# Kernel tuning notes

Hardware: AMD Instinct MI355X
Metric: run time of the kernel (lower is better)

The kernel has to match this reference:

```python
import jax, jax.numpy as jnp
import numpy as np

H = 1024        # hidden_size
NH = 16         # num_attention_heads
DH = H // NH    # head dim = 64
I = 4096        # intermediate_size
E = 8           # moe_num_experts
B, S = 2, 2048
EPS = 1e-12


def _ln(x, g, b):
    mu = jnp.mean(x, axis=-1, keepdims=True)
    var = jnp.mean(jnp.square(x - mu), axis=-1, keepdims=True)
    return (x - mu) * jax.lax.rsqrt(var + EPS) * g + b


def setup_inputs() -> dict:
    key = jax.random.key(0)
    ks = jax.random.split(key, 16)
    std = 0.02
    p = {
        "hidden_states": jax.random.normal(ks[0], (B, S, H), jnp.float32),
        "Wq": jax.random.normal(ks[1], (H, H), jnp.float32) * std,
        "bq": jnp.zeros((H,), jnp.float32),
        "Wk": jax.random.normal(ks[2], (H, H), jnp.float32) * std,
        "bk": jnp.zeros((H,), jnp.float32),
        "Wv": jax.random.normal(ks[3], (H, H), jnp.float32) * std,
        "bv": jnp.zeros((H,), jnp.float32),
        "Wao": jax.random.normal(ks[4], (H, H), jnp.float32) * std,
        "bao": jnp.zeros((H,), jnp.float32),
        "ln1_g": jnp.ones((H,), jnp.float32),
        "ln1_b": jnp.zeros((H,), jnp.float32),
        "router_w": jax.random.normal(ks[5], (H, E), jnp.float32) * std,
        "We": jax.random.normal(ks[6], (E, H, I), jnp.float32) * std,
        "be": jnp.zeros((E, I), jnp.float32),
        "Wo": jax.random.normal(ks[7], (I, H), jnp.float32) * std,
        "bo": jnp.zeros((H,), jnp.float32),
        "ln2_g": jnp.ones((H,), jnp.float32),
        "ln2_b": jnp.zeros((H,), jnp.float32),
    }
    return p


def reference(hidden_states, Wq, bq, Wk, bk, Wv, bv, Wao, bao, ln1_g, ln1_b,
              router_w, We, be, Wo, bo, ln2_g, ln2_b):
    x = hidden_states  # [B,S,H]

    def heads(t):  # [B,S,H] -> [B,NH,S,DH]
        return t.reshape(B, S, NH, DH).transpose(0, 2, 1, 3)

    q = heads(x @ Wq + bq)
    k = heads(x @ Wk + bk)
    v = heads(x @ Wv + bv)
    scores = jnp.einsum("bhqd,bhkd->bhqk", q, k) / jnp.sqrt(jnp.float32(DH))
    probs = jax.nn.softmax(scores, axis=-1)
    ctx = jnp.einsum("bhqk,bhkd->bhqd", probs, v)
    ctx = ctx.transpose(0, 2, 1, 3).reshape(B, S, H)
    attn_out = _ln(ctx @ Wao + bao + x, ln1_g, ln1_b)  # BertSelfOutput

    # ---- MoE FFN: top-1 routing, per-expert GELU MLP, shared output proj ----
    flat = attn_out.reshape(-1, H)              # [N,H]
    logits = flat @ router_w                    # [N,E]
    idx = jnp.argmax(logits, axis=-1)           # top-1 of softmax == argmax of logits
    inter = jnp.zeros((flat.shape[0], I), flat.dtype)
    for e in range(E):  # small fixed expert count
        h_e = jax.nn.gelu(flat @ We[e] + be[e], approximate=False)
        inter = jnp.where((idx == e)[:, None], h_e, inter)
    inter = inter.reshape(B, S, I)
    out = _ln(inter @ Wo + bo + attn_out, ln2_g, ln2_b)  # BertOutput
    return out
```

## Files before the change

### kernel.cpp

```cpp
#include <hip/hip_runtime.h>
#include <hip/hip_bf16.h>
#include <cstdint>

#define H_  1024
#define NH_ 16
#define DH_ 64
#define I_  4096
#define E_  8
#define B_  2
#define S_  2048
#define N_  4096
#define QKVLD 3072
#define LN_EPS 1e-12f

typedef __attribute__((ext_vector_type(4))) float f4;
typedef __attribute__((ext_vector_type(8))) short s8v;
typedef unsigned int u32;

__device__ __forceinline__ float bf2f(unsigned short u) {
  union { unsigned int i; float f; } c; c.i = ((unsigned int)u) << 16; return c.f;
}
__device__ __forceinline__ unsigned short f2bf(float f) {
  __hip_bfloat16 h = __float2bfloat16(f);
  return *reinterpret_cast<unsigned short*>(&h);
}
__device__ __forceinline__ u32 pack_bf2(float a, float b) {
  return (u32)f2bf(a) | ((u32)f2bf(b) << 16);
}
__device__ __forceinline__ float gelu_f(float x) {
  return 0.5f * x * (1.0f + erff(x * 0.70710678118f));
}
__device__ __forceinline__ void gload16(const void* g, void* l) {
  __builtin_amdgcn_global_load_lds(
      (const __attribute__((address_space(1))) void*)g,
      (__attribute__((address_space(3))) void*)l, 16, 0, 0);
}

__global__ __launch_bounds__(256) void cvt_bf16_kernel(
    const float* __restrict__ in, ushort* __restrict__ out, int n8)
{
  const int t = blockIdx.x * 256 + threadIdx.x;
  if (t >= n8) return;
  const f4 x0 = *(const f4*)(in + (size_t)t * 8);
  const f4 x1 = *(const f4*)(in + (size_t)t * 8 + 4);
  s8v o;
#pragma unroll
  for (int j = 0; j < 4; ++j) { o[j] = (short)f2bf(x0[j]); o[4 + j] = (short)f2bf(x1[j]); }
  *(s8v*)(out + (size_t)t * 8) = o;
}

__global__ __launch_bounds__(256) void transpose_cvt_kernel(
    const float* __restrict__ in, ushort* __restrict__ out, int R, int C)
{
  __shared__ float tile[32][33];
  const size_t zo = (size_t)blockIdx.z * R * C;
  const int bx = blockIdx.x << 5, by = blockIdx.y << 5;
  const int tx = threadIdx.x & 31, ty = threadIdx.x >> 5;
  const float* ip = in + zo + (size_t)by * C + bx;
#pragma unroll
  for (int i = 0; i < 4; ++i)
    tile[ty + 8 * i][tx] = ip[(size_t)(ty + 8 * i) * C + tx];
  __syncthreads();
  ushort* op = out + zo + (size_t)bx * R + by;
#pragma unroll
  for (int i = 0; i < 4; ++i)
    op[(size_t)(ty + 8 * i) * R + tx] = f2bf(tile[tx][ty + 8 * i]);
}

__global__ void concat3_kernel(const float* a, const float* b, const float* c,
                               float* __restrict__ o)
{
  const int t = blockIdx.x * 256 + threadIdx.x;
  if (t < 1024) o[t] = a[t];
  else if (t < 2048) o[t] = b[t - 1024];
  else o[t] = c[t - 2048];
}

__global__ __launch_bounds__(256) void gather_kernel(
    const ushort* __restrict__ X, const int* __restrict__ lists,
    ushort* __restrict__ Xg)
{
  const int r = (blockIdx.x << 1) + (threadIdx.x >> 7);
  const int c = (threadIdx.x & 127) << 3;
  const int tok = lists[r];
  *(s8v*)&Xg[(size_t)r * H_ + c] = *(const s8v*)&X[(size_t)tok * H_ + c];
}

template <bool BF16OUT, int KSPLIT>
__global__ __launch_bounds__(256, 4) void gemm_mfma_kernel(
    const ushort* __restrict__ A, const ushort* __restrict__ Bt,
    const float* __restrict__ bias, void* __restrict__ Cout,
    const int M, const int N, const int K)
{
  __shared__ __align__(16) ushort Asm[2][4][128][8];
  __shared__ __align__(16) ushort Bsm[2][4][128][8];
  const int tid = threadIdx.x;
  const int w = tid >> 6, l = tid & 63;
  const int lq = l & 15, g = l >> 4;
  const int wm = w >> 1, wn = w & 1;
  const int nbx = N >> 7;
  const int nwg = nbx * (M >> 7);
  int id = blockIdx.y * nbx + blockIdx.x;
  id = (id & 7) * (nwg >> 3) + (id >> 3);
  const int m0 = (id / nbx) << 7, n0 = (id % nbx) << 7;
  const int Kspan = K / KSPLIT;
  const int kbase = (KSPLIT > 1) ? blockIdx.z * Kspan : 0;

  const ushort* a0 = A + (size_t)(m0 + l) * K + kbase + (w << 3);
  const ushort* a1 = a0 + (size_t)64 * K;
  const ushort* b0 = Bt + (size_t)(n0 + l) * K + kbase + (w << 3);
  const ushort* b1 = b0 + (size_t)64 * K;

  f4 acc[4][4] = {};
  const int nt = Kspan >> 5;
#define STAGE_G(tt, buf)                                   \
  { const int kt_ = (tt) << 5;                             \
    gload16(a0 + kt_, &Asm[buf][w][0][0]);                 \
    gload16(a1 + kt_, &Asm[buf][w][64][0]);                \
    gload16(b0 + kt_, &Bsm[buf][w][0][0]);                 \
    gload16(b1 + kt_, &Bsm[buf][w][64][0]); }
  STAGE_G(0, 0);
  STAGE_G(1, 1);
  for (int t = 0; t < nt; ++t) {
    const int cur = t & 1;
    if (t + 1 < nt) { asm volatile("s_waitcnt vmcnt(4)" ::: "memory"); }
    else            { asm volatile("s_waitcnt vmcnt(0)" ::: "memory"); }
    __builtin_amdgcn_s_barrier();
    __builtin_amdgcn_sched_barrier(0);
    s8v af[4], bfv[4];
#pragma unroll
    for (int mi = 0; mi < 4; ++mi)
      af[mi] = *(const s8v*)&Asm[cur][g][(wm << 6) + (mi << 4) + lq][0];
#pragma unroll
    for (int ni = 0; ni < 4; ++ni)
      bfv[ni] = *(const s8v*)&Bsm[cur][g][(wn << 6) + (ni << 4) + lq][0];
    asm volatile("s_waitcnt lgkmcnt(0)" ::: "memory");
    __builtin_amdgcn_sched_barrier(0);
    __builtin_amdgcn_s_barrier();
    __builtin_amdgcn_sched_barrier(0);
    if (t + 2 < nt) STAGE_G(t + 2, cur);
#pragma unroll
    for (int mi = 0; mi < 4; ++mi)
#pragma unroll
      for (int ni = 0; ni < 4; ++ni)
        acc[mi][ni] = __builtin_amdgcn_mfma_f32_16x16x32_bf16(af[mi], bfv[ni], acc[mi][ni], 0, 0, 0);
  }
#undef STAGE_G
  if constexpr (BF16OUT) {
    ushort* st = (ushort*)Asm + (size_t)w * (16 * 72);
    float bs[4];
#pragma unroll
    for (int ni = 0; ni < 4; ++ni) bs[ni] = bias[n0 + (wn << 6) + (ni << 4) + lq];
#pragma unroll
    for (int mi = 0; mi < 4; ++mi) {
#pragma unroll
      for (int ni = 0; ni < 4; ++ni)
#pragma unroll
        for (int r = 0; r < 4; ++r)
          st[((g << 2) + r) * 72 + (ni << 4) + lq] = f2bf(acc[mi][ni][r] + bs[ni]);
#pragma unroll
      for (int q2 = 0; q2 < 2; ++q2) {
        const int r16 = l & 15, ch = (l >> 4) + (q2 << 2);
        const s8v vv = *(const s8v*)&st[r16 * 72 + (ch << 3)];
        *(s8v*)&((ushort*)Cout)[(size_t)(m0 + (wm << 6) + (mi << 4) + r16) * N
                                + n0 + (wn << 6) + (ch << 3)] = vv;
      }
    }
  } else {
    float* outf = (float*)Cout + (size_t)blockIdx.z * M * N;
#pragma unroll
    for (int ni = 0; ni < 4; ++ni) {
      const int col = n0 + (wn << 6) + (ni << 4) + lq;
      const float bs = (KSPLIT == 1 || blockIdx.z == 0) ? bias[col] : 0.f;
#pragma unroll
      for (int mi = 0; mi < 4; ++mi) {
        const int row = m0 + (wm << 6) + (mi << 4) + (g << 2);
#pragma unroll
        for (int r = 0; r < 4; ++r)
          outf[(size_t)(row + r) * N + col] = acc[mi][ni][r] + bs;
      }
    }
  }
}

__global__ __launch_bounds__(256, 4) void moe_mfma_kernel(
    const ushort* __restrict__ Xg, const ushort* __restrict__ WeT,
    const float* __restrict__ be, const int* __restrict__ lists,
    const int* __restrict__ offs, const int* __restrict__ cnt,
    const int* __restrict__ tb, ushort* __restrict__ inter)
{
  __shared__ __align__(16) ushort Asm[2][4][128][8];
  __shared__ __align__(16) ushort Bsm[2][4][128][8];
  __shared__ int tokL[128];
  const int by = blockIdx.y;
  if (by >= tb[E_]) return;
  int e = 0;
#pragma unroll
  for (int t = 1; t < E_; ++t) if (by >= tb[t]) e = t;
  const int rt = by - tb[e];
  const int base = offs[e] + (rt << 7);
  const int nrows = cnt[e] - (rt << 7);
  const int tid = threadIdx.x;
  if (tid < 128) tokL[tid] = (tid < nrows) ? lists[base + tid] : -1;
  __syncthreads();
  const int w = tid >> 6, l = tid & 63;
  const int lq = l & 15, g = l >> 4;
  const int wm = w >> 1, wn = w & 1;
  const int n0 = blockIdx.x << 7;
  const int r0 = min(base + l, N_ - 1);
  const int r1 = min(base + 64 + l, N_ - 1);
  const ushort* a0 = Xg + (size_t)r0 * H_ + (w << 3);
  const ushort* a1 = Xg + (size_t)r1 * H_ + (w << 3);
  const ushort* Wp = WeT + (size_t)e * I_ * H_;
  const ushort* b0 = Wp + (size_t)(n0 + l) * H_ + (w << 3);
  const ushort* b1 = b0 + (size_t)64 * H_;

  f4 acc[4][4] = {};
#define STAGE_M(tt, buf)                                   \
  { const int kt_ = (tt) << 5;                             \
    gload16(a0 + kt_, &Asm[buf][w][0][0]);                 \
    gload16(a1 + kt_, &Asm[buf][w][64][0]);                \
    gload16(b0 + kt_, &Bsm[buf][w][0][0]);                 \
    gload16(b1 + kt_, &Bsm[buf][w][64][0]); }
  STAGE_M(0, 0);
  STAGE_M(1, 1);
  for (int t = 0; t < 32; ++t) {
    const int cur = t & 1;
    if (t + 1 < 32) { asm volatile("s_waitcnt vmcnt(4)" ::: "memory"); }
    else            { asm volatile("s_waitcnt vmcnt(0)" ::: "memory"); }
    __builtin_amdgcn_s_barrier();
    __builtin_amdgcn_sched_barrier(0);
    s8v af[4], bfv[4];
#pragma unroll
    for (int mi = 0; mi < 4; ++mi)
      af[mi] = *(const s8v*)&Asm[cur][g][(wm << 6) + (mi << 4) + lq][0];
#pragma unroll
    for (int ni = 0; ni < 4; ++ni)
      bfv[ni] = *(const s8v*)&Bsm[cur][g][(wn << 6) + (ni << 4) + lq][0];
    asm volatile("s_waitcnt lgkmcnt(0)" ::: "memory");
    __builtin_amdgcn_sched_barrier(0);
    __builtin_amdgcn_s_barrier();
    __builtin_amdgcn_sched_barrier(0);
    if (t + 2 < 32) STAGE_M(t + 2, cur);
#pragma unroll
    for (int mi = 0; mi < 4; ++mi)
#pragma unroll
      for (int ni = 0; ni < 4; ++ni)
        acc[mi][ni] = __builtin_amdgcn_mfma_f32_16x16x32_bf16(af[mi], bfv[ni], acc[mi][ni], 0, 0, 0);
  }
#undef STAGE_M
  {
    ushort* st = (ushort*)Asm + (size_t)w * (16 * 72);
    float bs[4];
#pragma unroll
    for (int ni = 0; ni < 4; ++ni) bs[ni] = be[(size_t)e * I_ + n0 + (wn << 6) + (ni << 4) + lq];
#pragma unroll
    for (int mi = 0; mi < 4; ++mi) {
#pragma unroll
      for (int ni = 0; ni < 4; ++ni)
#pragma unroll
        for (int r = 0; r < 4; ++r)
          st[((g << 2) + r) * 72 + (ni << 4) + lq] = f2bf(gelu_f(acc[mi][ni][r] + bs[ni]));
#pragma unroll
      for (int q2 = 0; q2 < 2; ++q2) {
        const int r16 = l & 15, ch = (l >> 4) + (q2 << 2);
        const int tok = tokL[(wm << 6) + (mi << 4) + r16];
        if (tok >= 0) {
          const s8v vv = *(const s8v*)&st[r16 * 72 + (ch << 3)];
          *(s8v*)&inter[(size_t)tok * I_ + n0 + (wn << 6) + (ch << 3)] = vv;
        }
      }
    }
  }
}

__global__ __launch_bounds__(256) void attn_mfma_kernel(
    const ushort* __restrict__ qkv, ushort* __restrict__ ctx)
{
  __shared__ __align__(16) ushort Ks[64 * 72];
  __shared__ __align__(16) ushort Vt[64 * 72];
  __shared__ __align__(16) ushort Ps[4][16 * 72];
  const int bid0 = blockIdx.x;
  const int bid  = ((bid0 & 7) << 7) + (bid0 >> 3);
  const int bh = bid >> 5, qt = bid & 31;
  const int b = bh >> 4, h = bh & 15;
  const int tid = threadIdx.x, w = tid >> 6, l = tid & 63;
  const int lq = l & 15, g = l >> 4;
  const size_t bS = (size_t)b * S_;
  const ushort* qb = qkv + bS * QKVLD + h * DH_;
  const ushort* kb = qb + 1024;
  const ushort* vb = qb + 2048;

  s8v qf0, qf1;
  {
    const ushort* qp = qb + (size_t)(qt * 64 + w * 16 + lq) * QKVLD;
    qf0 = *(const s8v*)(qp + (g << 3));
    qf1 = *(const s8v*)(qp + 32 + (g << 3));
  }

  f4 o0 = {0,0,0,0}, o1 = {0,0,0,0}, o2 = {0,0,0,0}, o3 = {0,0,0,0};
  float mrun = -3.0e38f, lrun = 0.f;

  const int skey = tid >> 2;
  const int sd   = (tid & 3) << 4;

  for (int kt = 0; kt < 32; ++kt) {
    __syncthreads();
    {
      const ushort* kp = kb + (size_t)(kt * 64 + skey) * QKVLD + sd;
      *(s8v*)&Ks[skey * 72 + sd]     = *(const s8v*)(kp);
      *(s8v*)&Ks[skey * 72 + sd + 8] = *(const s8v*)(kp + 8);
      const ushort* vp = vb + (size_t)(kt * 64 + skey) * QKVLD + sd;
      const s8v v0 = *(const s8v*)(vp);
      const s8v v1 = *(const s8v*)(vp + 8);
#pragma unroll
      for (int ii = 0; ii < 8; ++ii) {
        Vt[(sd + ii) * 72 + skey]     = v0[ii];
        Vt[(sd + 8 + ii) * 72 + skey] = v1[ii];
      }
    }
    __syncthreads();

    float s[16];
#pragma unroll
    for (int st = 0; st < 4; ++st) {
      f4 acc = {0, 0, 0, 0};
      const s8v ka0 = *(const s8v*)&Ks[(st * 16 + lq) * 72 + (g << 3)];
      const s8v ka1 = *(const s8v*)&Ks[(st * 16 + lq) * 72 + 32 + (g << 3)];
      acc = __builtin_amdgcn_mfma_f32_16x16x32_bf16(ka0, qf0, acc, 0, 0, 0);
      acc = __builtin_amdgcn_mfma_f32_16x16x32_bf16(ka1, qf1, acc, 0, 0, 0);
      s[st * 4 + 0] = acc[0] * 0.125f; s[st * 4 + 1] = acc[1] * 0.125f;
      s[st * 4 + 2] = acc[2] * 0.125f; s[st * 4 + 3] = acc[3] * 0.125f;
    }

    float tmax = s[0];
#pragma unroll
    for (int i = 1; i < 16; ++i) tmax = fmaxf(tmax, s[i]);
    tmax = fmaxf(tmax, __shfl_xor(tmax, 16));
    tmax = fmaxf(tmax, __shfl_xor(tmax, 32));
    const float mnew  = fmaxf(mrun, tmax);
    const float alpha = __expf(mrun - mnew);
    float psum = 0.f;
#pragma unroll
    for (int i = 0; i < 16; ++i) { s[i] = __expf(s[i] - mnew); psum += s[i]; }
    psum += __shfl_xor(psum, 16); psum += __shfl_xor(psum, 32);
    lrun = lrun * alpha + psum; mrun = mnew;

    f4 av;
    av[0] = __shfl(alpha, g * 4 + 0); av[1] = __shfl(alpha, g * 4 + 1);
    av[2] = __shfl(alpha, g * 4 + 2); av[3] = __shfl(alpha, g * 4 + 3);
    o0 *= av; o1 *= av; o2 *= av; o3 *= av;

    {
      ushort* pw = &Ps[w][lq * 72];
#pragma unroll
      for (int st = 0; st < 4; ++st) {
        *(u32*)&pw[st * 16 + g * 4 + 0] = pack_bf2(s[st * 4 + 0], s[st * 4 + 1]);
        *(u32*)&pw[st * 16 + g * 4 + 2] = pack_bf2(s[st * 4 + 2], s[st * 4 + 3]);
      }
    }
    asm volatile("s_waitcnt lgkmcnt(0)" ::: "memory");
    __builtin_amdgcn_sched_barrier(0);

#pragma unroll
    for (int ks = 0; ks < 2; ++ks) {
      const int kof = ks * 32 + (g << 3);
      const s8v pa = *(const s8v*)&Ps[w][lq * 72 + kof];
      const s8v v0 = *(const s8v*)&Vt[( 0 + lq) * 72 + kof];
      const s8v v1 = *(const s8v*)&Vt[(16 + lq) * 72 + kof];
      const s8v v2 = *(const s8v*)&Vt[(32 + lq) * 72 + kof];
      const s8v v3 = *(const s8v*)&Vt[(48 + lq) * 72 + kof];
      o0 = __builtin_amdgcn_mfma_f32_16x16x32_bf16(pa, v0, o0, 0, 0, 0);
      o1 = __builtin_amdgcn_mfma_f32_16x16x32_bf16(pa, v1, o1, 0, 0, 0);
      o2 = __builtin_amdgcn_mfma_f32_16x16x32_bf16(pa, v2, o2, 0, 0, 0);
      o3 = __builtin_amdgcn_mfma_f32_16x16x32_bf16(pa, v3, o3, 0, 0, 0);
    }
  }

  const float inv = 1.f / lrun;
#pragma unroll
  for (int r = 0; r < 4; ++r) {
    const float li = __shfl(inv, g * 4 + r);
    ushort* op = ctx + (bS + (size_t)(qt * 64 + w * 16 + g * 4 + r)) * H_ + h * DH_ + lq;
    op[0]  = f2bf(o0[r] * li);
    op[16] = f2bf(o1[r] * li);
    op[32] = f2bf(o2[r] * li);
    op[48] = f2bf(o3[r] * li);
  }
}

template <int P>
__global__ __launch_bounds__(256) void add_ln_kernel(
    const float* __restrict__ a, const float* __restrict__ r,
    const float* __restrict__ g, const float* __restrict__ bta,
    float* __restrict__ out, ushort* __restrict__ ob)
{
  const int row = blockIdx.x, tid = threadIdx.x;
  const size_t base = (size_t)row * H_;
  const float4 xr = *(const float4*)(r + base + (tid << 2));
  float4 x = xr;
#pragma unroll
  for (int pp = 0; pp < P; ++pp) {
    const float4 xa = *(const float4*)(a + (size_t)pp * N_ * H_ + base + (tid << 2));
    x.x += xa.x; x.y += xa.y; x.z += xa.z; x.w += xa.w;
  }
  float s  = x.x + x.y + x.z + x.w;
  float ss = x.x * x.x + x.y * x.y + x.z * x.z + x.w * x.w;
#pragma unroll
  for (int off = 1; off < 64; off <<= 1) { s += __shfl_xor(s, off); ss += __shfl_xor(ss, off); }
  __shared__ float red[8];
  const int w = tid >> 6, ln = tid & 63;
  if (ln == 0) { red[w] = s; red[4 + w] = ss; }
  __syncthreads();
  const float S  = red[0] + red[1] + red[2] + red[3];
  const float SS = red[4] + red[5] + red[6] + red[7];
  const float mu  = S * (1.f / 1024.f);
  const float var = fmaxf(SS * (1.f / 1024.f) - mu * mu, 0.f);
  const float inv = rsqrtf(var + LN_EPS);
  const float4 gg = *(const float4*)&g[tid << 2];
  const float4 bb = *(const float4*)&bta[tid << 2];
  float4 y;
  y.x = (x.x - mu) * inv * gg.x + bb.x;
  y.y = (x.y - mu) * inv * gg.y + bb.y;
  y.z = (x.z - mu) * inv * gg.z + bb.z;
  y.w = (x.w - mu) * inv * gg.w + bb.w;
  *(float4*)&out[base + (tid << 2)] = y;
  if (ob) {
    ushort4 u;
    u.x = f2bf(y.x); u.y = f2bf(y.y); u.z = f2bf(y.z); u.w = f2bf(y.w);
    *(ushort4*)&ob[base + (tid << 2)] = u;
  }
}

__global__ __launch_bounds__(64) void router_kernel(
    const float* __restrict__ x, const float* __restrict__ rw,
    int* __restrict__ idx, int* __restrict__ cnt)
{
  const int t = blockIdx.x, lane = threadIdx.x;
  float acc[8] = {0.f};
  for (int c = 0; c < H_; c += 64) {
    const float xv = x[(size_t)t * H_ + c + lane];
    const float* wr = rw + (size_t)(c + lane) * E_;
    const float4 w0 = *(const float4*)wr;
    const float4 w1 = *(const float4*)(wr + 4);
    acc[0] += xv * w0.x; acc[1] += xv * w0.y; acc[2] += xv * w0.z; acc[3] += xv * w0.w;
    acc[4] += xv * w1.x; acc[5] += xv * w1.y; acc[6] += xv * w1.z; acc[7] += xv * w1.w;
  }
#pragma unroll
  for (int e = 0; e < E_; ++e) {
    float s = acc[e];
#pragma unroll
    for (int off = 1; off < 64; off <<= 1) s += __shfl_xor(s, off);
    acc[e] = s;
  }
  if (lane == 0) {
    int be_ = 0; float bv = acc[0];
#pragma unroll
    for (int e = 1; e < E_; ++e) if (acc[e] > bv) { bv = acc[e]; be_ = e; }
    idx[t] = be_;
    atomicAdd(&cnt[be_], 1);
  }
}

__global__ void init_kernel(int* cnt) { if (threadIdx.x < E_) cnt[threadIdx.x] = 0; }

__global__ void scan_kernel(const int* __restrict__ cnt, int* __restrict__ offs,
                            int* __restrict__ cursor, int* __restrict__ tb)
{
  int o = 0, tt = 0;
  for (int e = 0; e < E_; ++e) {
    offs[e] = o; cursor[e] = o; tb[e] = tt;
    o += cnt[e]; tt += (cnt[e] + 127) >> 7;
  }
  tb[E_] = tt;
}

__global__ __launch_bounds__(256) void scatter_kernel(
    const int* __restrict__ idx, int* __restrict__ cursor, int* __restrict__ lists)
{
  const int t = blockIdx.x * 256 + threadIdx.x;
  if (t < N_) {
    const int e = idx[t];
    const int p = atomicAdd(&cursor[e], 1);
    lists[p] = t;
  }
}

extern "C" void kernel_launch(void* const* d_in, const int* in_sizes, int n_in,
                              void* d_out, int out_size, void* d_ws, size_t ws_size,
                              hipStream_t stream) {
  const float* x   = (const float*)d_in[0];
  const float* Wq  = (const float*)d_in[1];
  const float* bq  = (const float*)d_in[2];
  const float* Wk  = (const float*)d_in[3];
  const float* bk  = (const float*)d_in[4];
  const float* Wv  = (const float*)d_in[5];
  const float* bv  = (const float*)d_in[6];
  const float* Wao = (const float*)d_in[7];
  const float* bao = (const float*)d_in[8];
  const float* g1  = (const float*)d_in[9];
  const float* b1  = (const float*)d_in[10];
  const float* rw  = (const float*)d_in[11];
  const float* We  = (const float*)d_in[12];
  const float* be  = (const float*)d_in[13];
  const float* Wo  = (const float*)d_in[14];
  const float* bo  = (const float*)d_in[15];
  const float* g2  = (const float*)d_in[16];
  const float* b2  = (const float*)d_in[17];
  float* out = (float*)d_out;

  char* p = (char*)d_ws;
  int* idx    = (int*)p; p += (size_t)N_ * 4;
  int* cnt    = (int*)p; p += 8 * 4;
  int* offs   = (int*)p; p += 8 * 4;
  int* cursor = (int*)p; p += 8 * 4;
  int* tb     = (int*)p; p += 16 * 4;
  int* lists  = (int*)p; p += (size_t)N_ * 4;
  p = (char*)(((uintptr_t)p + 255) & ~(uintptr_t)255);
  const size_t NH = (size_t)N_ * H_;
  ushort* xb     = (ushort*)p; p += NH * 2;
  ushort* qkvb   = (ushort*)p;
  float*  woPart = (float*)p;  p += (size_t)N_ * QKVLD * 2;
  ushort* ctxb   = (ushort*)p; p += NH * 2;
  float*  attn   = (float*)p;  p += NH * 4;
  ushort* attnb  = (ushort*)p; p += NH * 2;
  ushort* interb = (ushort*)p;
  float*  aoPart = (float*)p;  p += (size_t)N_ * I_ * 2;
  ushort* WqkvT  = (ushort*)p; p += (size_t)QKVLD * H_ * 2;
  ushort* WaoT   = (ushort*)p; p += (size_t)H_ * H_ * 2;
  ushort* WoT    = (ushort*)p; p += (size_t)H_ * I_ * 2;
  ushort* WeT    = (ushort*)p; p += (size_t)E_ * I_ * H_ * 2;
  float*  bqkv   = (float*)p;  p += QKVLD * 4;
  ushort* Xg     = xb;

  const dim3 blk(256);

  init_kernel<<<1, 64, 0, stream>>>(cnt);
  cvt_bf16_kernel<<<(N_ * H_ / 8 + 255) / 256, blk, 0, stream>>>(x, xb, N_ * H_ / 8);
  concat3_kernel<<<QKVLD / 256, blk, 0, stream>>>(bq, bk, bv, bqkv);
  transpose_cvt_kernel<<<dim3(32, 32, 1), blk, 0, stream>>>(Wq, WqkvT, H_, H_);
  transpose_cvt_kernel<<<dim3(32, 32, 1), blk, 0, stream>>>(Wk, WqkvT + (size_t)1024 * H_, H_, H_);
  transpose_cvt_kernel<<<dim3(32, 32, 1), blk, 0, stream>>>(Wv, WqkvT + (size_t)2048 * H_, H_, H_);
  transpose_cvt_kernel<<<dim3(32, 32, 1), blk, 0, stream>>>(Wao, WaoT, H_, H_);
  transpose_cvt_kernel<<<dim3(32, 128, 1), blk, 0, stream>>>(Wo, WoT, I_, H_);
  transpose_cvt_kernel<<<dim3(128, 32, 8), blk, 0, stream>>>(We, WeT, H_, I_);

  gemm_mfma_kernel<true, 1><<<dim3(QKVLD / 128, N_ / 128), blk, 0, stream>>>(
      xb, WqkvT, bqkv, qkvb, N_, QKVLD, H_);
  attn_mfma_kernel<<<1024, blk, 0, stream>>>(qkvb, ctxb);
  gemm_mfma_kernel<false, 2><<<dim3(H_ / 128, N_ / 128, 2), blk, 0, stream>>>(
      ctxb, WaoT, bao, aoPart, N_, H_, H_);
  add_ln_kernel<2><<<N_, blk, 0, stream>>>(aoPart, x, g1, b1, attn, attnb);
  router_kernel<<<N_, 64, 0, stream>>>(attn, rw, idx, cnt);
  scan_kernel<<<1, 1, 0, stream>>>(cnt, offs, cursor, tb);
  scatter_kernel<<<N_ / 256, blk, 0, stream>>>(idx, cursor, lists);
  gather_kernel<<<N_ / 2, blk, 0, stream>>>(attnb, lists, Xg);
  moe_mfma_kernel<<<dim3(I_ / 128, N_ / 128 + E_), blk, 0, stream>>>(
      Xg, WeT, be, lists, offs, cnt, tb, interb);
  gemm_mfma_kernel<false, 2><<<dim3(H_ / 128, N_ / 128, 2), blk, 0, stream>>>(
      interb, WoT, bo, woPart, N_, H_, I_);
  add_ln_kernel<2><<<N_, blk, 0, stream>>>(woPart, attn, g2, b2, out, (ushort*)nullptr);
}
```

Baseline: 523.4 us.

## Software-pipeline K/V loads in attention and skip unnecessary softmax rescaling

Restructures the attention inner loop so K/V tiles for step kt+2 are prefetched into registers and step kt+1 is written to LDS after the PV MFMAs, which overlaps global load latency with compute. V is first stored row-major and then transposed in LDS with vectorized stores, replacing the scattered 2-byte transposed writes. The online-softmax rescale is skipped when the new max exceeds the running max by at most 8, and s_setprio is raised around the MFMA sections. The lazy rescale can let exponentials reach e^8, which is tolerable in fp32 but slightly changes the bf16 P values. The barrier placement is also reworked and needs care to stay race-free.

```diff
diff --git a/kernel.cpp b/kernel.cpp
--- a/kernel.cpp
+++ b/kernel.cpp
@@ -278,6 +278,7 @@
     const ushort* __restrict__ qkv, ushort* __restrict__ ctx)
 {
   __shared__ __align__(16) ushort Ks[64 * 72];
+  __shared__ __align__(16) ushort Vr[64 * 72];
   __shared__ __align__(16) ushort Vt[64 * 72];
   __shared__ __align__(16) ushort Ps[4][16 * 72];
   const int bid0 = blockIdx.x;
@@ -304,24 +305,40 @@
   const int skey = tid >> 2;
   const int sd   = (tid & 3) << 4;
 
+  s8v kr0, kr1, vr0, vr1;
+#define ALOAD(t_) {                                                        \
+    const ushort* kp_ = kb + (size_t)((t_) * 64 + skey) * QKVLD + sd;      \
+    kr0 = *(const s8v*)kp_; kr1 = *(const s8v*)(kp_ + 8);                  \
+    const ushort* vp_ = vb + (size_t)((t_) * 64 + skey) * QKVLD + sd;      \
+    vr0 = *(const s8v*)vp_; vr1 = *(const s8v*)(vp_ + 8); }
+#define AWRITE() {                                                         \
+    *(s8v*)&Ks[skey * 72 + sd]     = kr0;                                  \
+    *(s8v*)&Ks[skey * 72 + sd + 8] = kr1;                                  \
+    *(s8v*)&Vr[skey * 72 + sd]     = vr0;                                  \
+    *(s8v*)&Vr[skey * 72 + sd + 8] = vr1; }
+
+  ALOAD(0); AWRITE();
+  ALOAD(1);
+
   for (int kt = 0; kt < 32; ++kt) {
-    __syncthreads();
+    asm volatile("s_waitcnt lgkmcnt(0)" ::: "memory");
+    __builtin_amdgcn_sched_barrier(0);
+    __builtin_amdgcn_s_barrier();
+    __builtin_amdgcn_sched_barrier(0);
+
     {
-      const ushort* kp = kb + (size_t)(kt * 64 + skey) * QKVLD + sd;
-      *(s8v*)&Ks[skey * 72 + sd]     = *(const s8v*)(kp);
-      *(s8v*)&Ks[skey * 72 + sd + 8] = *(const s8v*)(kp + 8);
-      const ushort* vp = vb + (size_t)(kt * 64 + skey) * QKVLD + sd;
-      const s8v v0 = *(const s8v*)(vp);
-      const s8v v1 = *(const s8v*)(vp + 8);
-#pragma unroll
-      for (int ii = 0; ii < 8; ++ii) {
-        Vt[(sd + ii) * 72 + skey]     = v0[ii];
-        Vt[(sd + 8 + ii) * 72 + skey] = v1[ii];
+      s8v t0, t1;
+#pragma unroll
+      for (int j = 0; j < 8; ++j) {
+        t0[j] = (short)Vr[(w * 16 + j) * 72 + l];
+        t1[j] = (short)Vr[(w * 16 + 8 + j) * 72 + l];
       }
-    }
-    __syncthreads();
+      *(s8v*)&Vt[l * 72 + w * 16]     = t0;
+      *(s8v*)&Vt[l * 72 + w * 16 + 8] = t1;
+    }
 
     float s[16];
+    __builtin_amdgcn_s_setprio(1);
 #pragma unroll
     for (int st = 0; st < 4; ++st) {
       f4 acc = {0, 0, 0, 0};
@@ -332,24 +349,27 @@
       s[st * 4 + 0] = acc[0] * 0.125f; s[st * 4 + 1] = acc[1] * 0.125f;
       s[st * 4 + 2] = acc[2] * 0.125f; s[st * 4 + 3] = acc[3] * 0.125f;
     }
+    __builtin_amdgcn_s_setprio(0);
 
     float tmax = s[0];
 #pragma unroll
     for (int i = 1; i < 16; ++i) tmax = fmaxf(tmax, s[i]);
     tmax = fmaxf(tmax, __shfl_xor(tmax, 16));
     tmax = fmaxf(tmax, __shfl_xor(tmax, 32));
-    const float mnew  = fmaxf(mrun, tmax);
-    const float alpha = __expf(mrun - mnew);
+    if (!__all(tmax - mrun <= 8.f)) {
+      const float mnew  = fmaxf(mrun, tmax);
+      const float alpha = __expf(mrun - mnew);
+      f4 av;
+      av[0] = __shfl(alpha, g * 4 + 0); av[1] = __shfl(alpha, g * 4 + 1);
+      av[2] = __shfl(alpha, g * 4 + 2); av[3] = __shfl(alpha, g * 4 + 3);
+      o0 *= av; o1 *= av; o2 *= av; o3 *= av;
+      lrun *= alpha; mrun = mnew;
+    }
     float psum = 0.f;
 #pragma unroll
-    for (int i = 0; i < 16; ++i) { s[i] = __expf(s[i] - mnew); psum += s[i]; }
+    for (int i = 0; i < 16; ++i) { s[i] = __expf(s[i] - mrun); psum += s[i]; }
     psum += __shfl_xor(psum, 16); psum += __shfl_xor(psum, 32);
-    lrun = lrun * alpha + psum; mrun = mnew;
-
-    f4 av;
-    av[0] = __shfl(alpha, g * 4 + 0); av[1] = __shfl(alpha, g * 4 + 1);
-    av[2] = __shfl(alpha, g * 4 + 2); av[3] = __shfl(alpha, g * 4 + 3);
-    o0 *= av; o1 *= av; o2 *= av; o3 *= av;
+    lrun += psum;
 
     {
       ushort* pw = &Ps[w][lq * 72];
@@ -361,7 +381,10 @@
     }
     asm volatile("s_waitcnt lgkmcnt(0)" ::: "memory");
     __builtin_amdgcn_sched_barrier(0);
-
+    __builtin_amdgcn_s_barrier();
+    __builtin_amdgcn_sched_barrier(0);
+
+    __builtin_amdgcn_s_setprio(1);
 #pragma unroll
     for (int ks = 0; ks < 2; ++ks) {
       const int kof = ks * 32 + (g << 3);
@@ -375,7 +398,13 @@
       o2 = __builtin_amdgcn_mfma_f32_16x16x32_bf16(pa, v2, o2, 0, 0, 0);
       o3 = __builtin_amdgcn_mfma_f32_16x16x32_bf16(pa, v3, o3, 0, 0, 0);
     }
-  }
+    __builtin_amdgcn_s_setprio(0);
+
+    if (kt + 1 < 32) AWRITE();
+    if (kt + 2 < 32) ALOAD(kt + 2);
+  }
+#undef ALOAD
+#undef AWRITE
 
   const float inv = 1.f / lrun;
 #pragma unroll
```

Measured after the change: 506.1 us. 1.03x faster.
